# Performance work log

Hardware: AMD Instinct MI355X
Metric: run time of the kernel (lower is better)

## Reference

```python
import jax, jax.numpy as jnp
import numpy as np

N = 50000
E = 800000
IN_DIM, HID, OUT = 64, 256, 128


def gcn_conv(x, edge_index, W, b):
    """PyG GCNConv with add_self_loops=False, sym normalization, unit edge weights.
    Transform-then-propagate: out[i] = sum_{e: col[e]=i} norm[e] * (x @ W)[row[e]] + b
    norm[e] = deg^-1/2[row] * deg^-1/2[col], deg = in-degree at col.
    """
    n = x.shape[0]
    row, col = edge_index[0], edge_index[1]
    xw = x @ W  # [N, out]
    deg = jax.ops.segment_sum(jnp.ones(row.shape[0], dtype=x.dtype), col, num_segments=n)
    dis = jnp.where(deg > 0, jax.lax.rsqrt(jnp.where(deg > 0, deg, 1.0)), 0.0)
    norm = dis[row] * dis[col]  # [E]
    msg = xw[row] * norm[:, None]  # [E, out]
    out = jax.ops.segment_sum(msg, col, num_segments=n)
    return out + b


def setup_inputs() -> dict:
    key = jax.random.key(0)
    ks = jax.random.split(key, 16)
    def lin(k, fi, fo):
        s = 1.0 / np.sqrt(fi)
        k1, k2 = jax.random.split(k)
        return (jax.random.uniform(k1, (fi, fo), jnp.float32, -s, s),
                jax.random.uniform(k2, (fo,), jnp.float32, -s, s))
    x = jax.random.normal(ks[0], (N, IN_DIM), jnp.float32)
    edge_index = jax.random.randint(ks[1], (2, E), 0, N, dtype=jnp.int64)
    w_fc, b_fc = lin(ks[2], IN_DIM, HID)
    w_conv1, b_conv1 = lin(ks[3], IN_DIM, HID)
    w_fc1, b_fc1 = lin(ks[4], 2 * HID, OUT)
    w_conv2, b_conv2 = lin(ks[5], 2 * HID, OUT)
    w_fc2, b_fc2 = lin(ks[6], OUT, 1)
    w_conv3, b_conv3 = lin(ks[7], OUT, 1)
    return dict(x=x, edge_index=edge_index,
                w_fc=w_fc, b_fc=b_fc, w_conv1=w_conv1, b_conv1=b_conv1,
                w_fc1=w_fc1, b_fc1=b_fc1, w_conv2=w_conv2, b_conv2=b_conv2,
                w_fc2=w_fc2, b_fc2=b_fc2, w_conv3=w_conv3, b_conv3=b_conv3)


def reference(x, edge_index, w_fc, b_fc, w_conv1, b_conv1, w_fc1, b_fc1,
              w_conv2, b_conv2, w_fc2, b_fc2, w_conv3, b_conv3):
    # MTGCL gcn_mlp, eval mode (dropout / dropout_adj are identity)
    x1 = jax.nn.relu(x @ w_fc + b_fc)                       # [N, HID]
    x2 = jax.nn.relu(gcn_conv(x, edge_index, w_conv1, b_conv1))  # [N, HID]
    x3 = jnp.concatenate((x1, x2), axis=1)                  # [N, 2*HID]
    x5 = jax.nn.relu(x3 @ w_fc1 + b_fc1)                    # [N, OUT]
    x6 = jax.nn.relu(gcn_conv(x3, edge_index, w_conv2, b_conv2))
    x7 = x5 + x6                                            # [N, OUT]
    pre = (x7 @ w_fc2 + b_fc2) + gcn_conv(x7, edge_index, w_conv3, b_conv3)
    return pre  # [N, 1]
```

## Files before the change

### kernel.cpp

```cpp
#include <hip/hip_runtime.h>
#include <hip/hip_bf16.h>

typedef __attribute__((ext_vector_type(8))) short short8;
typedef __attribute__((ext_vector_type(4))) float f32x4;

__device__ __forceinline__ ushort bf16_bits(float v) {
    __hip_bfloat16 h = __float2bfloat16(v);
    return *reinterpret_cast<ushort*>(&h);
}
__device__ __forceinline__ float bf16_val(float v) {
    __hip_bfloat16 h = __float2bfloat16(v);
    return __bfloat162float(h);
}
__device__ __forceinline__ float bfu_lo(uint u) {
    uint t = u << 16; return __uint_as_float(t);
}
__device__ __forceinline__ float bfu_hi(uint u) {
    uint t = u & 0xffff0000u; return __uint_as_float(t);
}


__global__ __launch_bounds__(256) void k_bcount(const int* __restrict__ col,
                                                int* __restrict__ bcnt, int E) {
    __shared__ int hist[196];
    int tid = threadIdx.x;
    int base = blockIdx.x * 2048;
    if (tid < 196) hist[tid] = 0;
    __syncthreads();
    #pragma unroll
    for (int i = 0; i < 8; i++) {
        int e = base + i * 256 + tid;
        if (e < E) atomicAdd(&hist[col[e] >> 8], 1);
    }
    __syncthreads();
    if (tid < 196 && hist[tid] > 0) atomicAdd(&bcnt[tid], hist[tid]);
}

__global__ __launch_bounds__(256) void k_bscan(const int* __restrict__ bcnt,
                                               int* __restrict__ bbase,
                                               int* __restrict__ bcur, int E) {
    int i = threadIdx.x;
    int v = (i < 196) ? bcnt[i] : 0;
    int lane = i & 63, w = i >> 6;
    int s = v;
    #pragma unroll
    for (int o = 1; o < 64; o <<= 1) {
        int t = __shfl_up(s, o);
        if (lane >= o) s += t;
    }
    __shared__ int wsum[4];
    if (lane == 63) wsum[w] = s;
    __syncthreads();
    int add = 0;
    for (int ww = 0; ww < w; ww++) add += wsum[ww];
    int excl = s + add - v;
    if (i < 196) {
        bbase[i] = excl;
        bcur[i] = excl;
    }
    if (i == 195) bbase[196] = excl + v;
}

__global__ __launch_bounds__(256) void k_binA(const int* __restrict__ row,
                                              const int* __restrict__ col,
                                              int* __restrict__ bcur,
                                              uint* __restrict__ stage, int E) {
    __shared__ uint colbuf[2048];
    __shared__ int hist[196];
    __shared__ int lcur[196];
    int tid = threadIdx.x;
    int base = blockIdx.x * 2048;
    if (tid < 196) hist[tid] = 0;
    __syncthreads();
    #pragma unroll
    for (int i = 0; i < 8; i++) {
        int e = base + i * 256 + tid;
        uint c = 0xFFFFFFFFu;
        if (e < E) {
            c = (uint)col[e];
            atomicAdd(&hist[c >> 8], 1);
        }
        colbuf[i * 256 + tid] = c;
    }
    __syncthreads();
    if (tid < 196 && hist[tid] > 0) lcur[tid] = atomicAdd(&bcur[tid], hist[tid]);
    __syncthreads();
    #pragma unroll
    for (int i = 0; i < 8; i++) {
        int idx = i * 256 + tid;
        uint c = colbuf[idx];
        if (c != 0xFFFFFFFFu) {
            uint r = (uint)row[base + idx];
            int p = atomicAdd(&lcur[c >> 8], 1);
            stage[p] = (c << 16) | r;
        }
    }
}

__global__ __launch_bounds__(256) void k_binB(const uint* __restrict__ stage,
                                              const int* __restrict__ bbase,
                                              int* __restrict__ rowptr,
                                              float* __restrict__ dis,
                                              ushort* __restrict__ csr16,
                                              int n, int E) {
    __shared__ int cnt[256];
    __shared__ int cur[256];
    __shared__ int wsum[4];
    int b = blockIdx.x;
    int lo = b << 8;
    int tid = threadIdx.x;
    int gstart = bbase[b], gend = bbase[b + 1];
    cnt[tid] = 0;
    __syncthreads();
    for (int idx = gstart + tid; idx < gend; idx += 256)
        atomicAdd(&cnt[(stage[idx] >> 16) & 255], 1);
    __syncthreads();
    int v = cnt[tid];
    int lane = tid & 63, w = tid >> 6;
    int s = v;
    #pragma unroll
    for (int o = 1; o < 64; o <<= 1) {
        int t = __shfl_up(s, o);
        if (lane >= o) s += t;
    }
    if (lane == 63) wsum[w] = s;
    __syncthreads();
    int add = 0;
    for (int ww = 0; ww < w; ww++) add += wsum[ww];
    int excl = s + add - v + gstart;
    int node = lo + tid;
    if (node < n) {
        rowptr[node] = excl;
        dis[node] = v > 0 ? rsqrtf((float)v) : 0.f;
    }
    cur[tid] = excl;
    if (tid == 0 && b == gridDim.x - 1) rowptr[n] = E;
    __syncthreads();
    for (int idx = gstart + tid; idx < gend; idx += 256) {
        uint pk = stage[idx];
        int p = atomicAdd(&cur[(pk >> 16) & 255], 1);
        csr16[p] = (ushort)(pk & 0xffffu);
    }
}


__global__ __launch_bounds__(256) void k_prepX(const float* __restrict__ x,
                                               const float* __restrict__ dis,
                                               ushort* __restrict__ xh,
                                               ushort* __restrict__ xs, int total4) {
    int i = blockIdx.x * 256 + threadIdx.x;
    if (i >= total4) return;
    float4 v = reinterpret_cast<const float4*>(x)[i];
    float dn = dis[i >> 4];
    float vv[4] = {v.x, v.y, v.z, v.w};
    uint hv[2], sv[2];
    #pragma unroll
    for (int g = 0; g < 2; g++) {
        float a0 = vv[g * 2], a1 = vv[g * 2 + 1];
        hv[g] = (uint)bf16_bits(a0) | ((uint)bf16_bits(a1) << 16);
        sv[g] = (uint)bf16_bits(a0 * dn) | ((uint)bf16_bits(a1 * dn) << 16);
    }
    reinterpret_cast<uint2*>(xh)[i] = make_uint2(hv[0], hv[1]);
    reinterpret_cast<uint2*>(xs)[i] = make_uint2(sv[0], sv[1]);
}


__global__ __launch_bounds__(256) void k_agg64_csr(const ushort* __restrict__ xs,
                                                   const int* __restrict__ rowptr,
                                                   const ushort* __restrict__ csr16,
                                                   const float* __restrict__ dis,
                                                   ushort* __restrict__ agghi, int n) {
    int node = blockIdx.x * 4 + (threadIdx.x >> 6);
    if (node >= n) return;
    int lane = threadIdx.x & 63;
    int sub = lane >> 3;
    int li  = lane & 7;
    int s = rowptr[node], t = rowptr[node + 1];
    float acc[8] = {};
    int p = s;
    for (; p + 16 <= t; p += 16) {
        int rr[2];
        #pragma unroll
        for (int u = 0; u < 2; u++) rr[u] = csr16[p + u * 8 + sub];
        uint4 v[2];
        #pragma unroll
        for (int u = 0; u < 2; u++)
            v[u] = *reinterpret_cast<const uint4*>(&xs[(size_t)rr[u] * 64 + li * 8]);
        #pragma unroll
        for (int u = 0; u < 2; u++) {
            acc[0] += bfu_lo(v[u].x); acc[1] += bfu_hi(v[u].x);
            acc[2] += bfu_lo(v[u].y); acc[3] += bfu_hi(v[u].y);
            acc[4] += bfu_lo(v[u].z); acc[5] += bfu_hi(v[u].z);
            acc[6] += bfu_lo(v[u].w); acc[7] += bfu_hi(v[u].w);
        }
    }
    for (; p < t; p += 8) {
        int e = p + sub;
        if (e < t) {
            int rr = csr16[e];
            uint4 v = *reinterpret_cast<const uint4*>(&xs[(size_t)rr * 64 + li * 8]);
            acc[0] += bfu_lo(v.x); acc[1] += bfu_hi(v.x);
            acc[2] += bfu_lo(v.y); acc[3] += bfu_hi(v.y);
            acc[4] += bfu_lo(v.z); acc[5] += bfu_hi(v.z);
            acc[6] += bfu_lo(v.w); acc[7] += bfu_hi(v.w);
        }
    }
    #pragma unroll
    for (int j = 0; j < 8; j++) {
        acc[j] += __shfl_xor(acc[j], 8);
        acc[j] += __shfl_xor(acc[j], 16);
        acc[j] += __shfl_xor(acc[j], 32);
    }
    if (sub == 0) {
        float dn = dis[node];
        uint hp[4];
        #pragma unroll
        for (int g = 0; g < 4; g++) {
            float a0 = acc[g * 2] * dn, a1 = acc[g * 2 + 1] * dn;
            hp[g] = (uint)bf16_bits(a0) | ((uint)bf16_bits(a1) << 16);
        }
        *reinterpret_cast<uint4*>(&agghi[(size_t)node * 64 + li * 8]) =
            make_uint4(hp[0], hp[1], hp[2], hp[3]);
    }
}

__global__ __launch_bounds__(256) void k_agg128_x7dot(
    const ushort* __restrict__ xw,
    const int* __restrict__ rowptr,
    const ushort* __restrict__ csr16,
    const float* __restrict__ dis,
    const float* __restrict__ b2,
    const ushort* __restrict__ x5,
    const float* __restrict__ wfc2, const float* __restrict__ bfc2,
    const float* __restrict__ wc3,  const float* __restrict__ bc3,
    float* __restrict__ out, float* __restrict__ xw3, int n) {
    int node = blockIdx.x * 4 + (threadIdx.x >> 6);
    if (node >= n) return;
    int lane = threadIdx.x & 63;
    int sub = lane >> 4;
    int li  = lane & 15;
    int s = rowptr[node], t = rowptr[node + 1];
    float acc[8] = {};
    int p = s;
    for (; p + 16 <= t; p += 16) {
        int rr[4];
        #pragma unroll
        for (int u = 0; u < 4; u++) rr[u] = csr16[p + u * 4 + sub];
        uint4 v[4];
        #pragma unroll
        for (int u = 0; u < 4; u++)
            v[u] = *reinterpret_cast<const uint4*>(&xw[(size_t)rr[u] * 128 + li * 8]);
        #pragma unroll
        for (int u = 0; u < 4; u++) {
            acc[0] += bfu_lo(v[u].x); acc[1] += bfu_hi(v[u].x);
            acc[2] += bfu_lo(v[u].y); acc[3] += bfu_hi(v[u].y);
            acc[4] += bfu_lo(v[u].z); acc[5] += bfu_hi(v[u].z);
            acc[6] += bfu_lo(v[u].w); acc[7] += bfu_hi(v[u].w);
        }
    }
    for (; p < t; p += 4) {
        int e = p + sub;
        if (e < t) {
            int rr = csr16[e];
            uint4 v = *reinterpret_cast<const uint4*>(&xw[(size_t)rr * 128 + li * 8]);
            acc[0] += bfu_lo(v.x); acc[1] += bfu_hi(v.x);
            acc[2] += bfu_lo(v.y); acc[3] += bfu_hi(v.y);
            acc[4] += bfu_lo(v.z); acc[5] += bfu_hi(v.z);
            acc[6] += bfu_lo(v.w); acc[7] += bfu_hi(v.w);
        }
    }
    #pragma unroll
    for (int j = 0; j < 8; j++) {
        acc[j] += __shfl_xor(acc[j], 16);
        acc[j] += __shfl_xor(acc[j], 32);
    }
    float dn = dis[node];
    float s1 = 0.f, s2 = 0.f;
    if (sub == 0) {
        uint4 xv = *reinterpret_cast<const uint4*>(&x5[(size_t)node * 128 + li * 8]);
        float xr[8] = {bfu_lo(xv.x), bfu_hi(xv.x), bfu_lo(xv.y), bfu_hi(xv.y),
                       bfu_lo(xv.z), bfu_hi(xv.z), bfu_lo(xv.w), bfu_hi(xv.w)};
        #pragma unroll
        for (int j = 0; j < 8; j++) {
            int d = li * 8 + j;
            float x7 = xr[j] + fmaxf(dn * acc[j] + b2[d], 0.f);
            s1 += x7 * wfc2[d];
            s2 += x7 * wc3[d];
        }
    }
    #pragma unroll
    for (int o = 32; o > 0; o >>= 1) {
        s1 += __shfl_down(s1, o);
        s2 += __shfl_down(s2, o);
    }
    if (lane == 0) {
        out[node] = s1 + bfc2[0] + bc3[0];
        xw3[node] = s2 * dn;
    }
}

__global__ __launch_bounds__(256) void k_agg1_csr(const float* __restrict__ sv,
                                                  const int* __restrict__ rowptr,
                                                  const ushort* __restrict__ csr16,
                                                  const float* __restrict__ dis,
                                                  float* __restrict__ out, int n) {
    int i = blockIdx.x * 256 + threadIdx.x;
    if (i >= n) return;
    int s = rowptr[i], t = rowptr[i + 1];
    float a = 0.f;
    #pragma unroll 4
    for (int p = s; p < t; ++p) a += sv[csr16[p]];
    out[i] += dis[i] * a;
}

__global__ __launch_bounds__(256) void k_prepW(const float* __restrict__ w0,
                                               const float* __restrict__ w1,
                                               const float* __restrict__ wf1,
                                               const float* __restrict__ wf2,
                                               ushort* __restrict__ W0f,
                                               ushort* __restrict__ W1f,
                                               ushort* __restrict__ Bf) {
    int id = blockIdx.x * 256 + threadIdx.x;
    if (id < 8192) {
        int mat = id >> 12;
        int rem = id & 4095;
        int lane = rem & 63;
        int nt = (rem >> 6) & 15;
        int k0i = (rem >> 10) & 1;
        int arr = rem >> 11;
        const float* w = mat ? w1 : w0;
        ushort* dst = mat ? W1f : W0f;
        int n = nt * 16 + (lane & 15);
        int kb = k0i * 32 + (lane >> 4) * 8;
        ushort o[8];
        #pragma unroll
        for (int j = 0; j < 8; j++) {
            float v = w[(size_t)(kb + j) * 256 + n];
            o[j] = arr ? bf16_bits(v - bf16_val(v)) : bf16_bits(v);
        }
        *reinterpret_cast<int4*>(&dst[(size_t)rem * 8]) = *reinterpret_cast<const int4*>(o);
    } else if (id < 24576) {
        int rem = id - 8192;
        int lane = rem & 63;
        int nt   = (rem >> 6) & 15;
        int k0i  = (rem >> 10) & 15;
        int n = nt * 16 + (lane & 15);
        int kbase = k0i * 32 + (lane >> 4) * 8;
        ushort outv[8];
        #pragma unroll
        for (int j = 0; j < 8; j++) {
            int k = kbase + j;
            float v = (n < 128) ? wf1[(size_t)k * 128 + n]
                                : wf2[(size_t)k * 128 + (n - 128)];
            outv[j] = bf16_bits(v);
        }
        *reinterpret_cast<int4*>(&Bf[(size_t)rem * 8]) = *reinterpret_cast<const int4*>(outv);
    }
}


__global__ __launch_bounds__(256) void k_mm64(
    const ushort* __restrict__ xh, const ushort* __restrict__ ah_,
    const ushort* __restrict__ W0f, const ushort* __restrict__ W1f,
    const float* __restrict__ b0, const float* __restrict__ b1,
    ushort* __restrict__ Af, int M) {
    const int layer = blockIdx.y;
    const ushort* A = layer ? ah_ : xh;
    const ushort* Wf = layer ? W1f : W0f;
    const float* bias = layer ? b1 : b0;
    const int colbase = layer * 256;

    const int t = threadIdx.x;
    const int lane = t & 63;
    const int wv = t >> 6;
    const int m0 = blockIdx.x * 64;
    const int ln15 = lane & 15;
    const int quad = lane >> 4;

    f32x4 acc[4][4] = {};

    #pragma unroll
    for (int k0i = 0; k0i < 2; k0i++) {
        short8 bh[4], bl[4];
        #pragma unroll
        for (int nt4 = 0; nt4 < 4; nt4++) {
            const ushort* pw = Wf + ((size_t)k0i * 16 + wv * 4 + nt4) * 512 + (size_t)lane * 8;
            bh[nt4] = *reinterpret_cast<const short8*>(pw);
            bl[nt4] = *reinterpret_cast<const short8*>(pw + 16384);
        }
        #pragma unroll
        for (int mt = 0; mt < 4; mt++) {
            int gm = m0 + mt * 16 + ln15;
            int gmc = gm < M - 1 ? gm : M - 1;
            size_t ia = (size_t)gmc * 64 + k0i * 32 + quad * 8;
            short8 a = *reinterpret_cast<const short8*>(&A[ia]);
            #pragma unroll
            for (int nt4 = 0; nt4 < 4; nt4++) {
                acc[mt][nt4] = __builtin_amdgcn_mfma_f32_16x16x32_bf16(a, bh[nt4], acc[mt][nt4], 0, 0, 0);
                acc[mt][nt4] = __builtin_amdgcn_mfma_f32_16x16x32_bf16(a, bl[nt4], acc[mt][nt4], 0, 0, 0);
            }
        }
    }

    #pragma unroll
    for (int mt = 0; mt < 4; mt++) {
        #pragma unroll
        for (int nt4 = 0; nt4 < 4; nt4++) {
            int gn = wv * 64 + nt4 * 16 + ln15;
            int gcol = gn + colbase;
            int k0f = gcol >> 5, qf = (gcol >> 3) & 3, j = gcol & 7;
            #pragma unroll
            for (int r = 0; r < 4; r++) {
                int gm = m0 + mt * 16 + quad * 4 + r;
                float v = fmaxf(acc[mt][nt4][r] + bias[gn], 0.f);
                size_t base = (((size_t)(gm >> 4)) * 16 + k0f) * 512 + (size_t)(qf * 16 + (gm & 15)) * 8 + j;
                Af[base] = bf16_bits(v);
            }
        }
    }
}

__global__ __launch_bounds__(256) void k_gemm2_mfma(
    const ushort* __restrict__ Af, const ushort* __restrict__ Bf,
    const float* __restrict__ bias1, const float* __restrict__ dis,
    ushort* __restrict__ C1, ushort* __restrict__ C2, int M) {
    const int t = threadIdx.x;
    const int lane = t & 63;
    const int wv = t >> 6;
    const int mt0 = blockIdx.x * 2;
    const int ln15 = lane & 15;
    const int quad = lane >> 4;

    f32x4 acc[2][4] = {};

    const ushort* aPtr = Af + ((size_t)mt0 * 16) * 512 + (size_t)lane * 8;
    const ushort* bPtr = Bf + ((size_t)wv * 4) * 512 + (size_t)lane * 8;

    short8 aC[2], bC[4];
    #pragma unroll
    for (int mt = 0; mt < 2; mt++)
        aC[mt] = *reinterpret_cast<const short8*>(aPtr + (size_t)mt * 16 * 512);
    #pragma unroll
    for (int nt = 0; nt < 4; nt++)
        bC[nt] = *reinterpret_cast<const short8*>(bPtr + (size_t)nt * 512);

    for (int k0i = 0; k0i < 16; k0i++) {
        short8 aN[2], bN[4];
        if (k0i < 15) {
            #pragma unroll
            for (int mt = 0; mt < 2; mt++)
                aN[mt] = *reinterpret_cast<const short8*>(aPtr + ((size_t)mt * 16 + k0i + 1) * 512);
            #pragma unroll
            for (int nt = 0; nt < 4; nt++)
                bN[nt] = *reinterpret_cast<const short8*>(bPtr + ((size_t)(k0i + 1) * 16 + nt) * 512);
        }
        #pragma unroll
        for (int mt = 0; mt < 2; mt++)
            #pragma unroll
            for (int nt = 0; nt < 4; nt++)
                acc[mt][nt] = __builtin_amdgcn_mfma_f32_16x16x32_bf16(aC[mt], bC[nt], acc[mt][nt], 0, 0, 0);
        if (k0i < 15) {
            #pragma unroll
            for (int mt = 0; mt < 2; mt++) aC[mt] = aN[mt];
            #pragma unroll
            for (int nt = 0; nt < 4; nt++) bC[nt] = bN[nt];
        }
    }

    #pragma unroll
    for (int mt = 0; mt < 2; mt++) {
        float dn[4];
        #pragma unroll
        for (int r = 0; r < 4; r++) {
            int gm = (mt0 + mt) * 16 + quad * 4 + r;
            dn[r] = (gm < M) ? dis[gm] : 0.f;
        }
        #pragma unroll
        for (int nt = 0; nt < 4; nt++) {
            int gn = wv * 64 + nt * 16 + ln15;
            #pragma unroll
            for (int r = 0; r < 4; r++) {
                int gm = (mt0 + mt) * 16 + quad * 4 + r;
                if (gm >= M) continue;
                float v = acc[mt][nt][r];
                if (gn < 128) {
                    C1[(size_t)gm * 128 + gn] = bf16_bits(fmaxf(v + bias1[gn], 0.f));
                } else {
                    C2[(size_t)gm * 128 + (gn - 128)] = bf16_bits(v * dn[r]);
                }
            }
        }
    }
}

extern "C" void kernel_launch(void* const* d_in, const int* in_sizes, int n_in,
                              void* d_out, int out_size, void* d_ws, size_t ws_size,
                              hipStream_t stream) {
    const float* x       = (const float*)d_in[0];
    const int*   ei      = (const int*)d_in[1];
    const float* w_fc    = (const float*)d_in[2];
    const float* b_fc    = (const float*)d_in[3];
    const float* w_conv1 = (const float*)d_in[4];
    const float* b_conv1 = (const float*)d_in[5];
    const float* w_fc1   = (const float*)d_in[6];
    const float* b_fc1   = (const float*)d_in[7];
    const float* w_conv2 = (const float*)d_in[8];
    const float* b_conv2 = (const float*)d_in[9];
    const float* w_fc2   = (const float*)d_in[10];
    const float* b_fc2   = (const float*)d_in[11];
    const float* w_conv3 = (const float*)d_in[12];
    const float* b_conv3 = (const float*)d_in[13];

    const int N = in_sizes[0] / 64;
    const int E = in_sizes[1] / 2;
    const int* row = ei;
    const int* col = ei + E;

    const int nb = (N + 255) / 256;
    const int nblk = (N + 63) / 64;
    const int nblk2 = (N + 31) / 32;
    const int Mt = nblk * 4;

    char* p = (char*)d_ws;
    auto alloc = [&](size_t elems) {
        void* q = p; p += ((elems + 3) & ~(size_t)3) * 4; return q;
    };
    int*    bcnt    = (int*)   alloc(200);
    int*    bbase   = (int*)   alloc(200);
    int*    bcur    = (int*)   alloc(200);
    int*    rowptr  = (int*)   alloc(N + 4);
    uint*   stage   = (uint*)  alloc(E);
    ushort* csr16   = (ushort*)alloc((size_t)E / 2);
    float*  dis     = (float*) alloc(N);
    ushort* xh      = (ushort*)alloc((size_t)N * 32);
    ushort* xs      = (ushort*)alloc((size_t)N * 32);
    ushort* agghi   = (ushort*)alloc((size_t)N * 32);
    ushort* x3f     = (ushort*)alloc((size_t)Mt * 4096);
    ushort* Bf      = (ushort*)alloc(65536);
    ushort* W0f     = (ushort*)alloc(16384);
    ushort* W1f     = (ushort*)alloc(16384);
    ushort* x5      = (ushort*)alloc((size_t)N * 64);
    ushort* xw2     = (ushort*)alloc((size_t)N * 64);
    float*  xw3     = (float*) alloc(N);

    float* out = (float*)d_out;

    hipMemsetAsync(bcnt, 0, 196 * sizeof(int), stream);
    k_bcount<<<(E + 2047) / 2048, 256, 0, stream>>>(col, bcnt, E);
    k_bscan<<<1, 256, 0, stream>>>(bcnt, bbase, bcur, E);
    k_binA<<<(E + 2047) / 2048, 256, 0, stream>>>(row, col, bcur, stage, E);
    k_binB<<<nb, 256, 0, stream>>>(stage, bbase, rowptr, dis, csr16, N, E);

    k_prepX<<<(N * 16 + 255) / 256, 256, 0, stream>>>(x, dis, xh, xs, N * 16);
    k_prepW<<<24576 / 256, 256, 0, stream>>>(w_fc, w_conv1, w_fc1, w_conv2,
                                             W0f, W1f, Bf);

    k_agg64_csr<<<(N + 3) / 4, 256, 0, stream>>>(xs, rowptr, csr16, dis, agghi, N);

    k_mm64<<<dim3(nblk, 2), 256, 0, stream>>>(xh, agghi, W0f, W1f,
                                              b_fc, b_conv1, x3f, N);

    k_gemm2_mfma<<<nblk2, 256, 0, stream>>>(x3f, Bf, b_fc1, dis, x5, xw2, N);

    k_agg128_x7dot<<<(N + 3) / 4, 256, 0, stream>>>(
        xw2, rowptr, csr16, dis, b_conv2, x5,
        w_fc2, b_fc2, w_conv3, b_conv3, out, xw3, N);

    k_agg1_csr<<<(N + 255) / 256, 256, 0, stream>>>(xw3, rowptr, csr16, dis, out, N);
}
```

Before: 268.6 us.

## Fuse first-layer GEMMs and second GEMM via swizzled LDS x3 tile

```diff
diff --git a/kernel.cpp b/kernel.cpp
--- a/kernel.cpp
+++ b/kernel.cpp
@@ -358,17 +358,18 @@
     }
 }
 
-
-__global__ __launch_bounds__(256) void k_mm64(
+__device__ __forceinline__ int x3_swz(int inner) {
+    return inner ^ ((((inner >> 6) & 1) << 4) ^ (((inner >> 7) & 1) << 3));
+}
+
+__global__ __launch_bounds__(256) void k_mmfused(
     const ushort* __restrict__ xh, const ushort* __restrict__ ah_,
     const ushort* __restrict__ W0f, const ushort* __restrict__ W1f,
     const float* __restrict__ b0, const float* __restrict__ b1,
-    ushort* __restrict__ Af, int M) {
-    const int layer = blockIdx.y;
-    const ushort* A = layer ? ah_ : xh;
-    const ushort* Wf = layer ? W1f : W0f;
-    const float* bias = layer ? b1 : b0;
-    const int colbase = layer * 256;
+    const ushort* __restrict__ Bf, const float* __restrict__ bias1,
+    const float* __restrict__ dis,
+    ushort* __restrict__ C1, ushort* __restrict__ C2, int M) {
+    __shared__ ushort x3[4 * 16 * 512];
 
     const int t = threadIdx.x;
     const int lane = t & 63;
@@ -377,110 +378,111 @@
     const int ln15 = lane & 15;
     const int quad = lane >> 4;
 
-    f32x4 acc[4][4] = {};
-
-    #pragma unroll
-    for (int k0i = 0; k0i < 2; k0i++) {
-        short8 bh[4], bl[4];
-        #pragma unroll
-        for (int nt4 = 0; nt4 < 4; nt4++) {
-            const ushort* pw = Wf + ((size_t)k0i * 16 + wv * 4 + nt4) * 512 + (size_t)lane * 8;
-            bh[nt4] = *reinterpret_cast<const short8*>(pw);
-            bl[nt4] = *reinterpret_cast<const short8*>(pw + 16384);
-        }
+    f32x4 acc[4][4];
+
+    #pragma unroll
+    for (int layer = 0; layer < 2; layer++) {
+        const ushort* A = layer ? ah_ : xh;
+        const ushort* Wf = layer ? W1f : W0f;
+        const float* bias = layer ? b1 : b0;
+        #pragma unroll
+        for (int mt = 0; mt < 4; mt++)
+            #pragma unroll
+            for (int nt4 = 0; nt4 < 4; nt4++)
+                acc[mt][nt4] = (f32x4){0.f, 0.f, 0.f, 0.f};
+
+        #pragma unroll
+        for (int k0i = 0; k0i < 2; k0i++) {
+            short8 bh[4], bl[4];
+            #pragma unroll
+            for (int nt4 = 0; nt4 < 4; nt4++) {
+                const ushort* pw = Wf + ((size_t)k0i * 16 + wv * 4 + nt4) * 512 + (size_t)lane * 8;
+                bh[nt4] = *reinterpret_cast<const short8*>(pw);
+                bl[nt4] = *reinterpret_cast<const short8*>(pw + 16384);
+            }
+            #pragma unroll
+            for (int mt = 0; mt < 4; mt++) {
+                int gm = m0 + mt * 16 + ln15;
+                int gmc = gm < M - 1 ? gm : M - 1;
+                size_t ia = (size_t)gmc * 64 + k0i * 32 + quad * 8;
+                short8 a = *reinterpret_cast<const short8*>(&A[ia]);
+                #pragma unroll
+                for (int nt4 = 0; nt4 < 4; nt4++) {
+                    acc[mt][nt4] = __builtin_amdgcn_mfma_f32_16x16x32_bf16(a, bh[nt4], acc[mt][nt4], 0, 0, 0);
+                    acc[mt][nt4] = __builtin_amdgcn_mfma_f32_16x16x32_bf16(a, bl[nt4], acc[mt][nt4], 0, 0, 0);
+                }
+            }
+        }
+
         #pragma unroll
         for (int mt = 0; mt < 4; mt++) {
-            int gm = m0 + mt * 16 + ln15;
-            int gmc = gm < M - 1 ? gm : M - 1;
-            size_t ia = (size_t)gmc * 64 + k0i * 32 + quad * 8;
-            short8 a = *reinterpret_cast<const short8*>(&A[ia]);
             #pragma unroll
             for (int nt4 = 0; nt4 < 4; nt4++) {
-                acc[mt][nt4] = __builtin_amdgcn_mfma_f32_16x16x32_bf16(a, bh[nt4], acc[mt][nt4], 0, 0, 0);
-                acc[mt][nt4] = __builtin_amdgcn_mfma_f32_16x16x32_bf16(a, bl[nt4], acc[mt][nt4], 0, 0, 0);
+                int gn = wv * 64 + nt4 * 16 + ln15;
+                int gcol = gn + layer * 256;
+                int k0f = gcol >> 5, qf = (gcol >> 3) & 3, j = gcol & 7;
+                #pragma unroll
+                for (int r = 0; r < 4; r++) {
+                    int rloc = quad * 4 + r;
+                    float v = fmaxf(acc[mt][nt4][r] + bias[gn], 0.f);
+                    int inner = x3_swz((qf * 16 + rloc) * 8 + j);
+                    x3[(mt * 16 + k0f) * 512 + inner] = bf16_bits(v);
+                }
             }
         }
     }
+    __syncthreads();
+
+    #pragma unroll
+    for (int mt = 0; mt < 4; mt++)
+        #pragma unroll
+        for (int nt = 0; nt < 4; nt++)
+            acc[mt][nt] = (f32x4){0.f, 0.f, 0.f, 0.f};
+
+    const int innerA = x3_swz(lane * 8);
+    const ushort* bPtr = Bf + ((size_t)wv * 4) * 512 + (size_t)lane * 8;
+
+    short8 bC[4];
+    #pragma unroll
+    for (int nt = 0; nt < 4; nt++)
+        bC[nt] = *reinterpret_cast<const short8*>(bPtr + (size_t)nt * 512);
+
+    for (int k0 = 0; k0 < 16; k0++) {
+        short8 bN[4];
+        if (k0 < 15) {
+            #pragma unroll
+            for (int nt = 0; nt < 4; nt++)
+                bN[nt] = *reinterpret_cast<const short8*>(bPtr + ((size_t)(k0 + 1) * 16 + nt) * 512);
+        }
+        short8 aF[4];
+        #pragma unroll
+        for (int mt = 0; mt < 4; mt++)
+            aF[mt] = *reinterpret_cast<const short8*>(&x3[(mt * 16 + k0) * 512 + innerA]);
+        #pragma unroll
+        for (int mt = 0; mt < 4; mt++)
+            #pragma unroll
+            for (int nt = 0; nt < 4; nt++)
+                acc[mt][nt] = __builtin_amdgcn_mfma_f32_16x16x32_bf16(aF[mt], bC[nt], acc[mt][nt], 0, 0, 0);
+        if (k0 < 15) {
+            #pragma unroll
+            for (int nt = 0; nt < 4; nt++) bC[nt] = bN[nt];
+        }
+    }
 
     #pragma unroll
     for (int mt = 0; mt < 4; mt++) {
-        #pragma unroll
-        for (int nt4 = 0; nt4 < 4; nt4++) {
-            int gn = wv * 64 + nt4 * 16 + ln15;
-            int gcol = gn + colbase;
-            int k0f = gcol >> 5, qf = (gcol >> 3) & 3, j = gcol & 7;
+        float dn[4];
+        #pragma unroll
+        for (int r = 0; r < 4; r++) {
+            int gm = m0 + mt * 16 + quad * 4 + r;
+            dn[r] = (gm < M) ? dis[gm] : 0.f;
+        }
+        #pragma unroll
+        for (int nt = 0; nt < 4; nt++) {
+            int gn = wv * 64 + nt * 16 + ln15;
             #pragma unroll
             for (int r = 0; r < 4; r++) {
                 int gm = m0 + mt * 16 + quad * 4 + r;
-                float v = fmaxf(acc[mt][nt4][r] + bias[gn], 0.f);
-                size_t base = (((size_t)(gm >> 4)) * 16 + k0f) * 512 + (size_t)(qf * 16 + (gm & 15)) * 8 + j;
-                Af[base] = bf16_bits(v);
-            }
-        }
-    }
-}
-
-__global__ __launch_bounds__(256) void k_gemm2_mfma(
-    const ushort* __restrict__ Af, const ushort* __restrict__ Bf,
-    const float* __restrict__ bias1, const float* __restrict__ dis,
-    ushort* __restrict__ C1, ushort* __restrict__ C2, int M) {
-    const int t = threadIdx.x;
-    const int lane = t & 63;
-    const int wv = t >> 6;
-    const int mt0 = blockIdx.x * 2;
-    const int ln15 = lane & 15;
-    const int quad = lane >> 4;
-
-    f32x4 acc[2][4] = {};
-
-    const ushort* aPtr = Af + ((size_t)mt0 * 16) * 512 + (size_t)lane * 8;
-    const ushort* bPtr = Bf + ((size_t)wv * 4) * 512 + (size_t)lane * 8;
-
-    short8 aC[2], bC[4];
-    #pragma unroll
-    for (int mt = 0; mt < 2; mt++)
-        aC[mt] = *reinterpret_cast<const short8*>(aPtr + (size_t)mt * 16 * 512);
-    #pragma unroll
-    for (int nt = 0; nt < 4; nt++)
-        bC[nt] = *reinterpret_cast<const short8*>(bPtr + (size_t)nt * 512);
-
-    for (int k0i = 0; k0i < 16; k0i++) {
-        short8 aN[2], bN[4];
-        if (k0i < 15) {
-            #pragma unroll
-            for (int mt = 0; mt < 2; mt++)
-                aN[mt] = *reinterpret_cast<const short8*>(aPtr + ((size_t)mt * 16 + k0i + 1) * 512);
-            #pragma unroll
-            for (int nt = 0; nt < 4; nt++)
-                bN[nt] = *reinterpret_cast<const short8*>(bPtr + ((size_t)(k0i + 1) * 16 + nt) * 512);
-        }
-        #pragma unroll
-        for (int mt = 0; mt < 2; mt++)
-            #pragma unroll
-            for (int nt = 0; nt < 4; nt++)
-                acc[mt][nt] = __builtin_amdgcn_mfma_f32_16x16x32_bf16(aC[mt], bC[nt], acc[mt][nt], 0, 0, 0);
-        if (k0i < 15) {
-            #pragma unroll
-            for (int mt = 0; mt < 2; mt++) aC[mt] = aN[mt];
-            #pragma unroll
-            for (int nt = 0; nt < 4; nt++) bC[nt] = bN[nt];
-        }
-    }
-
-    #pragma unroll
-    for (int mt = 0; mt < 2; mt++) {
-        float dn[4];
-        #pragma unroll
-        for (int r = 0; r < 4; r++) {
-            int gm = (mt0 + mt) * 16 + quad * 4 + r;
-            dn[r] = (gm < M) ? dis[gm] : 0.f;
-        }
-        #pragma unroll
-        for (int nt = 0; nt < 4; nt++) {
-            int gn = wv * 64 + nt * 16 + ln15;
-            #pragma unroll
-            for (int r = 0; r < 4; r++) {
-                int gm = (mt0 + mt) * 16 + quad * 4 + r;
                 if (gm >= M) continue;
                 float v = acc[mt][nt][r];
                 if (gn < 128) {
@@ -518,8 +520,6 @@
 
     const int nb = (N + 255) / 256;
     const int nblk = (N + 63) / 64;
-    const int nblk2 = (N + 31) / 32;
-    const int Mt = nblk * 4;
 
     char* p = (char*)d_ws;
     auto alloc = [&](size_t elems) {
@@ -535,7 +535,6 @@
     ushort* xh      = (ushort*)alloc((size_t)N * 32);
     ushort* xs      = (ushort*)alloc((size_t)N * 32);
     ushort* agghi   = (ushort*)alloc((size_t)N * 32);
-    ushort* x3f     = (ushort*)alloc((size_t)Mt * 4096);
     ushort* Bf      = (ushort*)alloc(65536);
     ushort* W0f     = (ushort*)alloc(16384);
     ushort* W1f     = (ushort*)alloc(16384);
@@ -557,10 +556,8 @@
 
     k_agg64_csr<<<(N + 3) / 4, 256, 0, stream>>>(xs, rowptr, csr16, dis, agghi, N);
 
-    k_mm64<<<dim3(nblk, 2), 256, 0, stream>>>(xh, agghi, W0f, W1f,
-                                              b_fc, b_conv1, x3f, N);
-
-    k_gemm2_mfma<<<nblk2, 256, 0, stream>>>(x3f, Bf, b_fc1, dis, x5, xw2, N);
+    k_mmfused<<<nblk, 256, 0, stream>>>(xh, agghi, W0f, W1f, b_fc, b_conv1,
+                                        Bf, b_fc1, dis, x5, xw2, N);
 
     k_agg128_x7dot<<<(N + 3) / 4, 256, 0, stream>>>(
         xw2, rowptr, csr16, dis, b_conv2, x5,
```

Result: faster. 250.2 us (-6.8%).
